# Kernel optimization log

Measured on AMD Instinct MI355X. Metric: run time of the kernel, lower is better.

## Reference

```python
import jax, jax.numpy as jnp
import numpy as np

B, S, D, P, R, NL = 16, 2048, 1024, 8192, 16, 64  # docs, seq, d_model, pairs, n_relations, n_label_pairs
MAX_SPAN = 32


def setup_inputs() -> dict:
    key = jax.random.key(0)
    ks = jax.random.split(key, 8)
    tokvecs = jax.random.normal(ks[0], (B, S, D), dtype=jnp.float32)
    batch_idx = jax.random.randint(ks[1], (P,), 0, B, dtype=jnp.int32)
    e1s = jax.random.randint(ks[2], (P,), 0, S - MAX_SPAN, dtype=jnp.int32)
    e1e = e1s + 1 + jax.random.randint(ks[3], (P,), 0, MAX_SPAN - 1, dtype=jnp.int32)
    e2s = jax.random.randint(ks[4], (P,), 0, S - MAX_SPAN, dtype=jnp.int32)
    e2e = e2s + 1 + jax.random.randint(ks[5], (P,), 0, MAX_SPAN - 1, dtype=jnp.int32)
    rel_idx = jax.random.randint(ks[6], (P,), 0, NL, dtype=jnp.int32)
    # multi-hot relationship-inclusion table (0/1 entries, as built in __init__)
    rel_table = (jax.random.uniform(ks[7], (NL, R)) < 0.25).astype(jnp.float32)
    return {
        "tokvecs": tokvecs,
        "batch_idx": batch_idx,
        "ent1_start": e1s,
        "ent1_end": e1e,
        "ent2_start": e2s,
        "ent2_end": e2e,
        "rel_idx": rel_idx,
        "rel_table": rel_table,
    }


def _span_mean(cs, b, s, e):
    # cs: [B, S+1, D] exclusive prefix sums; span mean = (cs[e] - cs[s]) / (e - s)
    seg = cs[b, e] - cs[b, s]                      # [P, D]
    return seg / (e - s)[:, None].astype(seg.dtype)


def reference(tokvecs, batch_idx, ent1_start, ent1_end, ent2_start, ent2_end, rel_idx, rel_table):
    Bn, Sn, Dn = tokvecs.shape
    # exclusive prefix sum along sequence -> O(1) mean per span instead of ragged gathers
    cs = jnp.concatenate(
        [jnp.zeros((Bn, 1, Dn), tokvecs.dtype), jnp.cumsum(tokvecs, axis=1)], axis=1
    )                                               # [B, S+1, D]
    m1 = _span_mean(cs, batch_idx, ent1_start, ent1_end)   # [P, D]
    m2 = _span_mean(cs, batch_idx, ent2_start, ent2_end)   # [P, D]
    rel = rel_table[rel_idx]                                # [P, R]
    return jnp.concatenate([m1, m2, rel], axis=-1)          # [P, 2D + R]
```

## Files before the change

### kernel.cpp

```cpp
#include <hip/hip_runtime.h>

#define S_LEN      2048
#define D_DIM      1024
#define R_DIM      16
#define OUT_STRIDE 2064
#define NKEYS      32768
#define GROUP      8


__global__ __launch_bounds__(256) void zero_hist(int* __restrict__ h) {
    h[blockIdx.x * 256 + threadIdx.x] = 0;
}

__global__ __launch_bounds__(256) void hist_jobs(
    const int* __restrict__ bidx, const int* __restrict__ e1s,
    const int* __restrict__ e2s, int* __restrict__ hist, int njobs)
{
    const int j = blockIdx.x * 256 + threadIdx.x;
    if (j >= njobs) return;
    const int p = j >> 1;
    const int s = (j & 1) ? e2s[p] : e1s[p];
    atomicAdd(hist + bidx[p] * S_LEN + s, 1);
}

__global__ __launch_bounds__(1024) void scan_hist(int* __restrict__ hist) {
    __shared__ int lds[1024];
    const int t = threadIdx.x;
    int v[32];
    int sum = 0;
#pragma unroll
    for (int i = 0; i < 32; ++i) { v[i] = hist[t * 32 + i]; sum += v[i]; }
    lds[t] = sum;
    __syncthreads();
    for (int off = 1; off < 1024; off <<= 1) {
        int x = (t >= off) ? lds[t - off] : 0;
        __syncthreads();
        lds[t] += x;
        __syncthreads();
    }
    int run = (t == 0) ? 0 : lds[t - 1];
#pragma unroll
    for (int i = 0; i < 32; ++i) { int c = v[i]; hist[t * 32 + i] = run; run += c; }
}

__global__ __launch_bounds__(256) void scatter_jobs(
    const int* __restrict__ bidx, const int* __restrict__ e1s,
    const int* __restrict__ e2s, int* __restrict__ cursor,
    int* __restrict__ sorted, int njobs)
{
    const int j = blockIdx.x * 256 + threadIdx.x;
    if (j >= njobs) return;
    const int p = j >> 1;
    const int s = (j & 1) ? e2s[p] : e1s[p];
    const int pos = atomicAdd(cursor + bidx[p] * S_LEN + s, 1);
    sorted[pos] = j;
}

__global__ __launch_bounds__(128) void gather_grouped3(
    const float* __restrict__ tok,
    const int*   __restrict__ sorted,
    const int*   __restrict__ bidx,
    const int*   __restrict__ e1s, const int* __restrict__ e1e,
    const int*   __restrict__ e2s, const int* __restrict__ e2e,
    const int*   __restrict__ ridx,
    const float* __restrict__ rtab,
    float*       __restrict__ out)
{
    const int blk = blockIdx.x;
    const int w  = (blk & 7) * (gridDim.x >> 3) + (blk >> 3);
    const int g  = w >> 1;
    const int ch = w & 1;
    const int t  = threadIdx.x;

    int   jp[GROUP], jh[GROUP], js[GROUP], je[GROUP];
    float jw[GROUP];
    int mins = 0x7fffffff, maxe = 0;
#pragma unroll
    for (int i = 0; i < GROUP; ++i) {
        const int id = __builtin_amdgcn_readfirstlane(sorted[g * GROUP + i]);
        const int p  = id >> 1;
        const int h  = id & 1;
        const int b  = __builtin_amdgcn_readfirstlane(bidx[p]);
        const int s  = __builtin_amdgcn_readfirstlane(h ? e2s[p] : e1s[p]);
        const int e  = __builtin_amdgcn_readfirstlane(h ? e2e[p] : e1e[p]);
        jp[i] = p; jh[i] = h;
        js[i] = b * S_LEN + s;
        je[i] = b * S_LEN + e;
        jw[i] = 1.0f / (float)(e - s);
        mins  = min(mins, js[i]);
        maxe  = max(maxe, je[i]);
    }

    float4 acc[GROUP];
#pragma unroll
    for (int i = 0; i < GROUP; ++i) acc[i] = make_float4(0.f, 0.f, 0.f, 0.f);

    const float4* base = reinterpret_cast<const float4*>(tok) +
                         (size_t)mins * (D_DIM / 4) + ch * 128 + t;
    const int nrows = maxe - mins;
    const int rmax  = nrows - 1;
    const int niter = (nrows + 3) >> 2;

    float4 cur[4];
#pragma unroll
    for (int k = 0; k < 4; ++k)
        cur[k] = base[(size_t)min(k, rmax) * (D_DIM / 4)];

    for (int it = 0; it < niter; ++it) {
        const int r0 = it * 4;
        float4 nxt[4];
#pragma unroll
        for (int k = 0; k < 4; ++k)
            nxt[k] = base[(size_t)min(r0 + 4 + k, rmax) * (D_DIM / 4)];

        const int gr = mins + r0;
#pragma unroll
        for (int i = 0; i < GROUP; ++i) {
            const float w0 = (gr + 0 >= js[i] && gr + 0 < je[i]) ? jw[i] : 0.f;
            const float w1 = (gr + 1 >= js[i] && gr + 1 < je[i]) ? jw[i] : 0.f;
            const float w2 = (gr + 2 >= js[i] && gr + 2 < je[i]) ? jw[i] : 0.f;
            const float w3 = (gr + 3 >= js[i] && gr + 3 < je[i]) ? jw[i] : 0.f;
            acc[i].x += cur[0].x * w0 + cur[1].x * w1 + cur[2].x * w2 + cur[3].x * w3;
            acc[i].y += cur[0].y * w0 + cur[1].y * w1 + cur[2].y * w2 + cur[3].y * w3;
            acc[i].z += cur[0].z * w0 + cur[1].z * w1 + cur[2].z * w2 + cur[3].z * w3;
            acc[i].w += cur[0].w * w0 + cur[1].w * w1 + cur[2].w * w2 + cur[3].w * w3;
        }
#pragma unroll
        for (int k = 0; k < 4; ++k) cur[k] = nxt[k];
    }

#pragma unroll
    for (int i = 0; i < GROUP; ++i) {
        float* dst = out + (size_t)jp[i] * OUT_STRIDE + jh[i] * D_DIM +
                     ch * 512 + t * 4;
        *reinterpret_cast<float4*>(dst) = acc[i];
        if (ch == 0 && jh[i] == 0 && t < 4) {
            const float4 rv = *reinterpret_cast<const float4*>(
                rtab + ridx[jp[i]] * R_DIM + t * 4);
            *reinterpret_cast<float4*>(
                out + (size_t)jp[i] * OUT_STRIDE + 2 * D_DIM + t * 4) = rv;
        }
    }
}

extern "C" void kernel_launch(void* const* d_in, const int* in_sizes, int n_in,
                              void* d_out, int out_size, void* d_ws, size_t ws_size,
                              hipStream_t stream) {
    const float* tok  = (const float*)d_in[0];
    const int*   bidx = (const int*)d_in[1];
    const int*   e1s  = (const int*)d_in[2];
    const int*   e1e  = (const int*)d_in[3];
    const int*   e2s  = (const int*)d_in[4];
    const int*   e2e  = (const int*)d_in[5];
    const int*   ridx = (const int*)d_in[6];
    const float* rtab = (const float*)d_in[7];
    float*       out  = (float*)d_out;

    const int P     = in_sizes[1];
    const int njobs = 2 * P;

    int* cursor = (int*)d_ws;
    int* sorted = (int*)d_ws + NKEYS;

    zero_hist<<<NKEYS / 256, 256, 0, stream>>>(cursor);
    hist_jobs<<<(njobs + 255) / 256, 256, 0, stream>>>(bidx, e1s, e2s, cursor, njobs);
    scan_hist<<<1, 1024, 0, stream>>>(cursor);
    scatter_jobs<<<(njobs + 255) / 256, 256, 0, stream>>>(bidx, e1s, e2s, cursor,
                                                          sorted, njobs);
    const int nblocks = (njobs / GROUP) * 2;
    gather_grouped3<<<nblocks, 128, 0, stream>>>(
        tok, sorted, bidx, e1s, e1e, e2s, e2e, ridx, rtab, out);
}
```

Before: 266.8 us.

## Fuse job sorting into one single-block LDS kernel and shrink gather group

Replaces the four-kernel global-memory histogram sort (zero, histogram, scan, scatter) with one single-workgroup kernel. It does a counting sort in shared memory over coarser buckets (four start positions per bucket), which removes three launches and the global atomics. The gather group size also drops from 8 to 4, doubling the block count and cutting the per-block span union and the registers held in accumulators. The risks are that one workgroup now serially processes all 16K jobs with LDS atomics, and that smaller groups reuse fewer shared token rows, raising global read traffic.

```diff
diff --git a/kernel.cpp b/kernel.cpp
--- a/kernel.cpp
+++ b/kernel.cpp
@@ -4,59 +4,55 @@
 #define D_DIM      1024
 #define R_DIM      16
 #define OUT_STRIDE 2064
-#define NKEYS      32768
-#define GROUP      8
+#define NBUCK      8192
+#define BPT        8
+#define GROUP      4
 
+__global__ __launch_bounds__(1024) void sort_jobs(
+    const int* __restrict__ bidx, const int* __restrict__ e1s,
+    const int* __restrict__ e2s, int* __restrict__ sorted, int njobs)
+{
+    __shared__ int hist[NBUCK];
+    __shared__ int part[1024];
+    const int t = threadIdx.x;
 
-__global__ __launch_bounds__(256) void zero_hist(int* __restrict__ h) {
-    h[blockIdx.x * 256 + threadIdx.x] = 0;
+#pragma unroll
+    for (int i = 0; i < BPT; ++i) hist[t * BPT + i] = 0;
+    __syncthreads();
+
+    for (int j = t; j < njobs; j += 1024) {
+        const int p = j >> 1;
+        const int s = (j & 1) ? e2s[p] : e1s[p];
+        atomicAdd(&hist[(bidx[p] * S_LEN + s) >> 2], 1);
+    }
+    __syncthreads();
+
+    int v[BPT];
+    int sum = 0;
+#pragma unroll
+    for (int i = 0; i < BPT; ++i) { v[i] = hist[t * BPT + i]; sum += v[i]; }
+    part[t] = sum;
+    __syncthreads();
+    for (int off = 1; off < 1024; off <<= 1) {
+        int x = (t >= off) ? part[t - off] : 0;
+        __syncthreads();
+        part[t] += x;
+        __syncthreads();
+    }
+    int run = (t == 0) ? 0 : part[t - 1];
+#pragma unroll
+    for (int i = 0; i < BPT; ++i) { int c = v[i]; hist[t * BPT + i] = run; run += c; }
+    __syncthreads();
+
+    for (int j = t; j < njobs; j += 1024) {
+        const int p = j >> 1;
+        const int s = (j & 1) ? e2s[p] : e1s[p];
+        const int pos = atomicAdd(&hist[(bidx[p] * S_LEN + s) >> 2], 1);
+        sorted[pos] = j;
+    }
 }
 
-__global__ __launch_bounds__(256) void hist_jobs(
-    const int* __restrict__ bidx, const int* __restrict__ e1s,
-    const int* __restrict__ e2s, int* __restrict__ hist, int njobs)
-{
-    const int j = blockIdx.x * 256 + threadIdx.x;
-    if (j >= njobs) return;
-    const int p = j >> 1;
-    const int s = (j & 1) ? e2s[p] : e1s[p];
-    atomicAdd(hist + bidx[p] * S_LEN + s, 1);
-}
-
-__global__ __launch_bounds__(1024) void scan_hist(int* __restrict__ hist) {
-    __shared__ int lds[1024];
-    const int t = threadIdx.x;
-    int v[32];
-    int sum = 0;
-#pragma unroll
-    for (int i = 0; i < 32; ++i) { v[i] = hist[t * 32 + i]; sum += v[i]; }
-    lds[t] = sum;
-    __syncthreads();
-    for (int off = 1; off < 1024; off <<= 1) {
-        int x = (t >= off) ? lds[t - off] : 0;
-        __syncthreads();
-        lds[t] += x;
-        __syncthreads();
-    }
-    int run = (t == 0) ? 0 : lds[t - 1];
-#pragma unroll
-    for (int i = 0; i < 32; ++i) { int c = v[i]; hist[t * 32 + i] = run; run += c; }
-}
-
-__global__ __launch_bounds__(256) void scatter_jobs(
-    const int* __restrict__ bidx, const int* __restrict__ e1s,
-    const int* __restrict__ e2s, int* __restrict__ cursor,
-    int* __restrict__ sorted, int njobs)
-{
-    const int j = blockIdx.x * 256 + threadIdx.x;
-    if (j >= njobs) return;
-    const int p = j >> 1;
-    const int s = (j & 1) ? e2s[p] : e1s[p];
-    const int pos = atomicAdd(cursor + bidx[p] * S_LEN + s, 1);
-    sorted[pos] = j;
-}
-
-__global__ __launch_bounds__(128) void gather_grouped3(
+__global__ __launch_bounds__(128) void gather_g4(
     const float* __restrict__ tok,
     const int*   __restrict__ sorted,
     const int*   __restrict__ bidx,
@@ -159,15 +155,11 @@
     const int P     = in_sizes[1];
     const int njobs = 2 * P;
 
-    int* cursor = (int*)d_ws;
-    int* sorted = (int*)d_ws + NKEYS;
+    int* sorted = (int*)d_ws;
 
-    zero_hist<<<NKEYS / 256, 256, 0, stream>>>(cursor);
-    hist_jobs<<<(njobs + 255) / 256, 256, 0, stream>>>(bidx, e1s, e2s, cursor, njobs);
-    scan_hist<<<1, 1024, 0, stream>>>(cursor);
-    scatter_jobs<<<(njobs + 255) / 256, 256, 0, stream>>>(bidx, e1s, e2s, cursor,
-                                                          sorted, njobs);
+    sort_jobs<<<1, 1024, 0, stream>>>(bidx, e1s, e2s, sorted, njobs);
+
     const int nblocks = (njobs / GROUP) * 2;
-    gather_grouped3<<<nblocks, 128, 0, stream>>>(
+    gather_g4<<<nblocks, 128, 0, stream>>>(
         tok, sorted, bidx, e1s, e1e, e2s, e2e, ridx, rtab, out);
 }
```

Measured after the change: 268.1 us. No clear change (+0.5%).
